# Kernel tuning notes

Measured on AMD Instinct MI355X. Metric: run time of the kernel, lower is better.

The kernel has to match this reference:

```python
import jax, jax.numpy as jnp
import numpy as np

SEQ, BATCH, IN, HID = 512, 64, 1024, 1024

def setup_inputs() -> dict:
    key = jax.random.key(0)
    k1, k2, k3 = jax.random.split(key, 3)
    X = jax.random.normal(k1, (SEQ, BATCH, IN), dtype=jnp.float32)
    hidden_state = jnp.zeros((BATCH, HID), dtype=jnp.float32)
    # nn.Linear(in, out, bias=False) weight has shape [out, in]
    W = jax.random.normal(k2, (HID, IN), dtype=jnp.float32) / np.sqrt(IN)
    H = jax.random.normal(k3, (HID, HID), dtype=jnp.float32) / np.sqrt(HID)
    return {"X": X, "hidden_state": hidden_state, "W": W, "H": H}

def reference(X, hidden_state, W, H):
    # Faithful to the torch code: hidden_state is NEVER updated inside the loop
    # (the module uses `hidden_state`, not `out`, each step), so
    #   out_t = tanh(X_t @ W^T + hidden_state @ H^T)   for every t,
    # and the H-term is constant across time. This vectorizes exactly.
    h_term = hidden_state @ H.T                      # [B, HID]
    output = jnp.tanh(jnp.einsum('tbi,hi->tbh', X, W) + h_term[None, :, :])  # [T,B,HID]
    return (output, output[-1])
```

## Files before the change

kernel.cpp:

```cpp
#include <hip/hip_runtime.h>


typedef __bf16 bf16x8 __attribute__((ext_vector_type(8)));
typedef float f32x4 __attribute__((ext_vector_type(4)));
typedef unsigned short us4 __attribute__((ext_vector_type(4)));

constexpr int M_TOT = 32768;
constexpr int K_D = 1024;
constexpr int N_D = 1024;
constexpr int NTK = K_D / 32;

__device__ __forceinline__ void async16(const void* g, void* l) {
  __builtin_amdgcn_global_load_lds(
      (const __attribute__((address_space(1))) unsigned int*)g,
      (__attribute__((address_space(3))) unsigned int*)l, 16, 0, 0);
}

__device__ __forceinline__ unsigned short f2bf(float f) {
  unsigned int u = __float_as_uint(f);
  u += 0x7FFFu + ((u >> 16) & 1u);
  return (unsigned short)(u >> 16);
}

constexpr int PREP_XBLK = M_TOT * K_D / 4 / 256;
constexpr int PREP_WBLK = N_D * K_D / 4 / 256;
constexpr int PREP_HBLK = 1024;
constexpr int PREP_GRID = PREP_XBLK + PREP_WBLK + PREP_HBLK;

__global__ __launch_bounds__(256) void prep_kernel(
    const float* __restrict__ X, unsigned short* __restrict__ Xbf,
    const float* __restrict__ W, unsigned short* __restrict__ Wbf,
    const float* __restrict__ hs, const float* __restrict__ Hm,
    float* __restrict__ ht) {
  __shared__ float4 Hrow4[256];
  const int b = blockIdx.x;
  const int tid = threadIdx.x;

  if (b < PREP_XBLK + PREP_WBLK) {
    const float* in = (b < PREP_XBLK) ? X : W;
    unsigned short* out = (b < PREP_XBLK) ? Xbf : Wbf;
    int j = (b < PREP_XBLK) ? (b * 256 + tid) : ((b - PREP_XBLK) * 256 + tid);
    int slot = j >> 1, half = j & 1;
    int row = slot >> 7, st = slot & 127;
    int sd = (st & ~3) | ((st & 3) ^ ((row >> 1) & 3));
    float4 a = *reinterpret_cast<const float4*>(in + (size_t)j * 4);
    us4 v;
    v[0] = f2bf(a.x); v[1] = f2bf(a.y); v[2] = f2bf(a.z); v[3] = f2bf(a.w);
    *reinterpret_cast<us4*>(out + (size_t)row * 1024 + sd * 8 + half * 4) = v;
  } else {
    int h = b - (PREP_XBLK + PREP_WBLK);
    Hrow4[tid] = reinterpret_cast<const float4*>(Hm + (size_t)h * 1024)[tid];
    __syncthreads();
    int w = tid >> 6, l = tid & 63;
#pragma unroll 2
    for (int bb = w * 16; bb < w * 16 + 16; ++bb) {
      const float4* hb4 = reinterpret_cast<const float4*>(hs + (size_t)bb * 1024);
      float s = 0.f;
#pragma unroll
      for (int p = 0; p < 4; ++p) {
        float4 x = hb4[l + p * 64];
        float4 y = Hrow4[l + p * 64];
        s += x.x * y.x + x.y * y.y + x.z * y.z + x.w * y.w;
      }
#pragma unroll
      for (int off = 32; off > 0; off >>= 1) s += __shfl_down(s, off, 64);
      if (l == 0) ht[bb * 1024 + h] = s;
    }
  }
}

__global__ __launch_bounds__(256, 4) void gemm_tanh(
    const unsigned short* __restrict__ A, const unsigned short* __restrict__ B,
    const float* __restrict__ ht, float* __restrict__ out0,
    float* __restrict__ out1) {
  __shared__ unsigned short As[2][128 * 32];
  __shared__ unsigned short Bs[2][128 * 32];

  int bid = blockIdx.x;
  int swz = (bid & 7) * 256 + (bid >> 3);
  int bm = swz >> 3;
  int bn = swz & 7;

  int tid = threadIdx.x;
  int lane = tid & 63, wid = tid >> 6;
  int wr = wid >> 1, wc = wid & 1;
  int fr = lane & 15, kq = lane >> 4;

  int c1 = tid + 256;
  const unsigned short* gA0 =
      A + (size_t)(bm * 128 + (tid >> 2)) * 1024 + (tid & 3) * 8;
  const unsigned short* gA1 =
      A + (size_t)(bm * 128 + (c1 >> 2)) * 1024 + (c1 & 3) * 8;
  const unsigned short* gB0 =
      B + (size_t)(bn * 128 + (tid >> 2)) * 1024 + (tid & 3) * 8;
  const unsigned short* gB1 =
      B + (size_t)(bn * 128 + (c1 >> 2)) * 1024 + (c1 & 3) * 8;

  f32x4 acc[4][4] = {};

#define STAGE(kt, buf)                                \
  {                                                   \
    async16(gA0 + (kt) * 32, &As[buf][tid * 8]);      \
    async16(gA1 + (kt) * 32, &As[buf][c1 * 8]);       \
    async16(gB0 + (kt) * 32, &Bs[buf][tid * 8]);      \
    async16(gB1 + (kt) * 32, &Bs[buf][c1 * 8]);       \
  }

  STAGE(0, 0);
  asm volatile("s_waitcnt vmcnt(0)" ::: "memory");
  __builtin_amdgcn_s_barrier();
  asm volatile("" ::: "memory");

  for (int kt = 0; kt < NTK; ++kt) {
    const int cur = kt & 1;
    if (kt + 1 < NTK) STAGE(kt + 1, cur ^ 1);

    bf16x8 af[4], bg[4];
#pragma unroll
    for (int mi = 0; mi < 4; ++mi) {
      int ra = wr * 64 + mi * 16 + fr;
      af[mi] = *reinterpret_cast<const bf16x8*>(
          &As[cur][ra * 32 + (kq ^ ((ra >> 1) & 3)) * 8]);
    }
#pragma unroll
    for (int ni = 0; ni < 4; ++ni) {
      int rb = wc * 64 + ni * 16 + fr;
      bg[ni] = *reinterpret_cast<const bf16x8*>(
          &Bs[cur][rb * 32 + (kq ^ ((rb >> 1) & 3)) * 8]);
    }
#pragma unroll
    for (int mi = 0; mi < 4; ++mi)
#pragma unroll
      for (int ni = 0; ni < 4; ++ni)
        acc[mi][ni] = __builtin_amdgcn_mfma_f32_16x16x32_bf16(
            af[mi], bg[ni], acc[mi][ni], 0, 0, 0);

    if (kt + 1 < NTK) {
      asm volatile("s_waitcnt vmcnt(0)" ::: "memory");
      __builtin_amdgcn_s_barrier();
      asm volatile("" ::: "memory");
    }
  }

  const int nbase = bn * 128 + wc * 64;
#pragma unroll
  for (int mi = 0; mi < 4; ++mi) {
#pragma unroll
    for (int r = 0; r < 4; ++r) {
      int mloc = wr * 64 + mi * 16 + kq * 4 + r;
      size_t m = (size_t)bm * 128 + mloc;
      int b = mloc & 63;
#pragma unroll
      for (int ni = 0; ni < 4; ++ni) {
        int n = nbase + ni * 16 + fr;
        float x = acc[mi][ni][r] + ht[b * 1024 + n];
        float e = __expf(2.0f * x);
        float y = 1.0f - 2.0f / (e + 1.0f);
        out0[m * 1024 + n] = y;
        if (m >= (size_t)(M_TOT - 64))
          out1[(m - (M_TOT - 64)) * 1024 + n] = y;
      }
    }
  }
#undef STAGE
}

extern "C" void kernel_launch(void* const* d_in, const int* in_sizes, int n_in,
                              void* d_out, int out_size, void* d_ws,
                              size_t ws_size, hipStream_t stream) {
  (void)in_sizes; (void)n_in; (void)out_size; (void)ws_size;
  const float* X  = (const float*)d_in[0];
  const float* hs = (const float*)d_in[1];
  const float* W  = (const float*)d_in[2];
  const float* Hm = (const float*)d_in[3];
  float* out0 = (float*)d_out;
  float* out1 = out0 + (size_t)M_TOT * N_D;

  unsigned short* Xbf = (unsigned short*)d_ws;
  unsigned short* Wbf = Xbf + (size_t)M_TOT * K_D;
  float* hterm = (float*)(Wbf + (size_t)N_D * K_D);

  prep_kernel<<<PREP_GRID, 256, 0, stream>>>(X, Xbf, W, Wbf, hs, Hm, hterm);
  gemm_tanh<<<(M_TOT / 128) * (N_D / 128), 256, 0, stream>>>(Xbf, Wbf, hterm,
                                                             out0, out1);
}
```

Measured before the change: 161.0 us.

## Load B fragments directly from global and triple-buffer A tile in LDS

The W operand is now stored in plain row-major bf16 and each wave loads its B fragments straight from global memory into registers, skipping LDS for B. A is staged through a three-deep LDS ring with two tiles in flight, and waits use vmcnt(2) instead of a full drain. MFMA issue is also wrapped in raised wave priority. This aims to cut LDS traffic and barrier stalls, at the cost of uncoalesced per-lane global loads for B, and the vmcnt counts now have to cover those B loads too.

Result: slower. 217.0 us (+34.8%).

```diff
diff --git a/kernel.cpp b/kernel.cpp
--- a/kernel.cpp
+++ b/kernel.cpp
@@ -36,17 +36,21 @@
   const int b = blockIdx.x;
   const int tid = threadIdx.x;
 
-  if (b < PREP_XBLK + PREP_WBLK) {
-    const float* in = (b < PREP_XBLK) ? X : W;
-    unsigned short* out = (b < PREP_XBLK) ? Xbf : Wbf;
-    int j = (b < PREP_XBLK) ? (b * 256 + tid) : ((b - PREP_XBLK) * 256 + tid);
+  if (b < PREP_XBLK) {
+    int j = b * 256 + tid;
     int slot = j >> 1, half = j & 1;
     int row = slot >> 7, st = slot & 127;
     int sd = (st & ~3) | ((st & 3) ^ ((row >> 1) & 3));
-    float4 a = *reinterpret_cast<const float4*>(in + (size_t)j * 4);
+    float4 a = *reinterpret_cast<const float4*>(X + (size_t)j * 4);
     us4 v;
     v[0] = f2bf(a.x); v[1] = f2bf(a.y); v[2] = f2bf(a.z); v[3] = f2bf(a.w);
-    *reinterpret_cast<us4*>(out + (size_t)row * 1024 + sd * 8 + half * 4) = v;
+    *reinterpret_cast<us4*>(Xbf + (size_t)row * 1024 + sd * 8 + half * 4) = v;
+  } else if (b < PREP_XBLK + PREP_WBLK) {
+    int j = (b - PREP_XBLK) * 256 + tid;
+    float4 a = *reinterpret_cast<const float4*>(W + (size_t)j * 4);
+    us4 v;
+    v[0] = f2bf(a.x); v[1] = f2bf(a.y); v[2] = f2bf(a.z); v[3] = f2bf(a.w);
+    *reinterpret_cast<us4*>(Wbf + (size_t)j * 4) = v;
   } else {
     int h = b - (PREP_XBLK + PREP_WBLK);
     Hrow4[tid] = reinterpret_cast<const float4*>(Hm + (size_t)h * 1024)[tid];
@@ -73,8 +77,7 @@
     const unsigned short* __restrict__ A, const unsigned short* __restrict__ B,
     const float* __restrict__ ht, float* __restrict__ out0,
     float* __restrict__ out1) {
-  __shared__ unsigned short As[2][128 * 32];
-  __shared__ unsigned short Bs[2][128 * 32];
+  __shared__ unsigned short As[3][128 * 32];
 
   int bid = blockIdx.x;
   int swz = (bid & 7) * 256 + (bid >> 3);
@@ -91,52 +94,57 @@
       A + (size_t)(bm * 128 + (tid >> 2)) * 1024 + (tid & 3) * 8;
   const unsigned short* gA1 =
       A + (size_t)(bm * 128 + (c1 >> 2)) * 1024 + (c1 & 3) * 8;
-  const unsigned short* gB0 =
-      B + (size_t)(bn * 128 + (tid >> 2)) * 1024 + (tid & 3) * 8;
-  const unsigned short* gB1 =
-      B + (size_t)(bn * 128 + (c1 >> 2)) * 1024 + (c1 & 3) * 8;
+  const unsigned short* gBf =
+      B + (size_t)(bn * 128 + wc * 64 + fr) * 1024 + kq * 8;
 
   f32x4 acc[4][4] = {};
 
-#define STAGE(kt, buf)                                \
+#define STAGE_A(kt, buf)                              \
   {                                                   \
     async16(gA0 + (kt) * 32, &As[buf][tid * 8]);      \
     async16(gA1 + (kt) * 32, &As[buf][c1 * 8]);       \
-    async16(gB0 + (kt) * 32, &Bs[buf][tid * 8]);      \
-    async16(gB1 + (kt) * 32, &Bs[buf][c1 * 8]);       \
   }
 
-  STAGE(0, 0);
-  asm volatile("s_waitcnt vmcnt(0)" ::: "memory");
+  STAGE_A(0, 0);
+  STAGE_A(1, 1);
+  asm volatile("s_waitcnt vmcnt(2)" ::: "memory");
   __builtin_amdgcn_s_barrier();
   asm volatile("" ::: "memory");
 
   for (int kt = 0; kt < NTK; ++kt) {
-    const int cur = kt & 1;
-    if (kt + 1 < NTK) STAGE(kt + 1, cur ^ 1);
+    const int cur = kt % 3;
+    const int ks = kt * 32;
 
-    bf16x8 af[4], bg[4];
+    bf16x8 bg[4];
+#pragma unroll
+    for (int ni = 0; ni < 4; ++ni)
+      bg[ni] = *reinterpret_cast<const bf16x8*>(gBf + (size_t)ni * 16 * 1024 + ks);
+    asm volatile("" ::: "memory");
+
+    if (kt + 2 < NTK) STAGE_A(kt + 2, (kt + 2) % 3);
+
+    bf16x8 af[4];
 #pragma unroll
     for (int mi = 0; mi < 4; ++mi) {
       int ra = wr * 64 + mi * 16 + fr;
       af[mi] = *reinterpret_cast<const bf16x8*>(
           &As[cur][ra * 32 + (kq ^ ((ra >> 1) & 3)) * 8]);
     }
-#pragma unroll
-    for (int ni = 0; ni < 4; ++ni) {
-      int rb = wc * 64 + ni * 16 + fr;
-      bg[ni] = *reinterpret_cast<const bf16x8*>(
-          &Bs[cur][rb * 32 + (kq ^ ((rb >> 1) & 3)) * 8]);
-    }
+
+    __builtin_amdgcn_s_setprio(1);
 #pragma unroll
     for (int mi = 0; mi < 4; ++mi)
 #pragma unroll
       for (int ni = 0; ni < 4; ++ni)
         acc[mi][ni] = __builtin_amdgcn_mfma_f32_16x16x32_bf16(
             af[mi], bg[ni], acc[mi][ni], 0, 0, 0);
+    __builtin_amdgcn_s_setprio(0);
 
     if (kt + 1 < NTK) {
-      asm volatile("s_waitcnt vmcnt(0)" ::: "memory");
+      if (kt + 2 < NTK)
+        asm volatile("s_waitcnt vmcnt(2)" ::: "memory");
+      else
+        asm volatile("s_waitcnt vmcnt(0)" ::: "memory");
       __builtin_amdgcn_s_barrier();
       asm volatile("" ::: "memory");
     }
@@ -162,7 +170,7 @@
       }
     }
   }
-#undef STAGE
+#undef STAGE_A
 }
 
 extern "C" void kernel_launch(void* const* d_in, const int* in_sizes, int n_in,
```
